# Optimization experiments

Measured on AMD Instinct MI355X. Metric: run time of the kernel, lower is better.

The kernel has to match this reference:

```python
import jax, jax.numpy as jnp
import numpy as np

N, IN_DIM, HID, E = 2048, 128, 64, 32768
EPS = 1e-5  # torch BatchNorm1d / LayerNorm default eps


def setup_inputs() -> dict:
    key = jax.random.key(0)
    ks = jax.random.split(key, 12)
    s = 0.05
    return {
        "h": jax.random.normal(ks[0], (N, IN_DIM), jnp.float32),
        "local": jax.random.normal(ks[1], (N, IN_DIM), jnp.float32),
        "e": jax.random.normal(ks[2], (E, HID), jnp.float32),
        "src": jax.random.randint(ks[3], (E,), 0, N, jnp.int32),
        "dst": jax.random.randint(ks[4], (E,), 0, N, jnp.int32),
        "ln_w": jnp.ones((IN_DIM,), jnp.float32),
        "ln_b": jnp.zeros((IN_DIM,), jnp.float32),
        "conv_w": jax.random.normal(ks[5], (1, 2, 3), jnp.float32) * 0.3,
        "conv_b": jnp.zeros((1,), jnp.float32),
        "W1": jax.random.normal(ks[6], (IN_DIM, HID * HID), jnp.float32) * s,
        "b1": jnp.zeros((HID * HID,), jnp.float32),
        "Wp2": jax.random.normal(ks[7], (IN_DIM, HID), jnp.float32) * s,
        "bp2": jnp.zeros((HID,), jnp.float32),
        "W2": jax.random.normal(ks[8], (IN_DIM, HID), jnp.float32) * s,
        "b2": jnp.zeros((HID,), jnp.float32),
        "W3": jax.random.normal(ks[9], (HID, HID), jnp.float32) * s,
        "b3": jnp.zeros((HID,), jnp.float32),
        "bng_g": jnp.ones((HID,), jnp.float32),
        "bng_b": jnp.zeros((HID,), jnp.float32),
        "bnG_g": jnp.ones((HID,), jnp.float32),
        "bnG_b": jnp.zeros((HID,), jnp.float32),
        "bnL_g": jnp.ones((HID,), jnp.float32),
        "bnL_b": jnp.zeros((HID,), jnp.float32),
    }


def _bn_eval(x, g, b):
    # BatchNorm1d in eval mode, running_mean=0, running_var=1
    return x * (g / jnp.sqrt(1.0 + EPS)) + b


def _layernorm(x, w, b):
    mu = jnp.mean(x, axis=-1, keepdims=True)
    var = jnp.var(x, axis=-1, keepdims=True)
    return (x - mu) / jnp.sqrt(var + EPS) * w + b


def reference(h, local, e, src, dst, ln_w, ln_b, conv_w, conv_b,
              W1, b1, Wp2, bp2, W2, b2, W3, b3,
              bng_g, bng_b, bnG_g, bnG_b, bnL_g, bnL_b):
    # ---- local edge branch ----
    edge = jnp.stack([local[src], local[dst]], axis=1)  # [E, 2, in_dim]
    edge = _layernorm(edge, ln_w, ln_b)
    # Conv1d(2 -> 1, k=3, pad=1) over the in_dim axis
    lr_local = jax.lax.conv_general_dilated(
        edge, conv_w, window_strides=(1,), padding=[(1, 1)],
        dimension_numbers=("NCH", "OIH", "NCH"))[:, 0, :] + conv_b  # [E, in_dim]
    lr_local = jax.nn.relu(lr_local)  # dropout is identity in eval
    lr_local = lr_local @ W2 + b2  # [E, hid]

    # ---- global edge branch ----
    p1 = jax.nn.relu(h @ W1 + b1).reshape(h.shape[0], HID, HID)  # [N, hid(d), hid(k)]
    p2 = jax.nn.relu(h @ Wp2 + bp2)  # [N, hid(k)]
    # mm[i, j, d] = sum_k p1[i, d, k] * p2[j, k]; gather only needed edges
    lr_global = jnp.einsum("edk,ek->ed", p1[src], p2[dst])  # [E, hid]
    lr_global = _bn_eval(lr_global, bng_g, bng_b) @ W3 + b3
    lr_global = jax.nn.relu(_bn_eval(lr_global, bnG_g, bnG_b))

    lr_local = jax.nn.relu(_bn_eval(lr_local, bnL_g, bnL_b))
    return lr_local + lr_global + e
```

## Files before the change

### kernel.cpp

```cpp
#include <hip/hip_runtime.h>

#define N_NODES 2048
#define IN_DIM 128
#define HID 64
#define N_EDGES 32768
#define EPS 1e-5f
#define CAP 64
#define TPN 4
#define NTILES (N_NODES * TPN)
#define POISON ((int)0xAAAAAAAA)

typedef short short8 __attribute__((ext_vector_type(8)));
typedef float f32x4 __attribute__((ext_vector_type(4)));

__device__ __forceinline__ float relu_f(float x) { return fmaxf(x, 0.f); }

__device__ __forceinline__ unsigned short f2bf(float f) {
  unsigned int u = __float_as_uint(f);
  u = (u + 0x7fffu + ((u >> 16) & 1u)) >> 16;
  return (unsigned short)u;
}
__device__ __forceinline__ float bf2f(unsigned short h) {
  return __uint_as_float(((unsigned int)h) << 16);
}
__device__ __forceinline__ short8 pack8(const float* f) {
  short8 o;
  #pragma unroll
  for (int i = 0; i < 8; ++i) o[i] = (short)f2bf(f[i]);
  return o;
}

__global__ __launch_bounds__(256) void gemm_prep(
    const float* __restrict__ h, const float* __restrict__ local,
    const float* __restrict__ ln_w, const float* __restrict__ ln_b,
    const float* __restrict__ Wp2, const float* __restrict__ bp2,
    const float* __restrict__ W1, const float* __restrict__ b1,
    const float* __restrict__ W2, const float* __restrict__ W3,
    const int* __restrict__ src, const int* __restrict__ dst,
    unsigned short* __restrict__ p1b, unsigned short* __restrict__ lnlb,
    unsigned short* __restrict__ p2b,
    unsigned short* __restrict__ w2tb, unsigned short* __restrict__ w3tb,
    int* __restrict__ cursor, int2* __restrict__ slot_ed)
{
  __shared__ __align__(16) struct { float hs[4][IN_DIM]; } S;
  const int b = blockIdx.x, t = threadIdx.x;
  const int w = t >> 6, l = t & 63;
  const int lr = l & 15, lq = l >> 4;

  if (b < 1024) {
    const int bm = (b & 31) * 64;
    const int bn = (b >> 5) * 128;
    const int m0 = bm + w * 16;
    f32x4 acc[8];
    #pragma unroll
    for (int ni = 0; ni < 8; ++ni) acc[ni] = (f32x4){0.f, 0.f, 0.f, 0.f};

    #pragma unroll
    for (int k0 = 0; k0 < 128; k0 += 32) {
      const float* hrow = h + (size_t)(m0 + lr) * 128 + k0 + lq * 8;
      float4 h0 = *(const float4*)hrow;
      float4 h1 = *(const float4*)(hrow + 4);
      short8 bmf;
      bmf[0] = (short)f2bf(h0.x); bmf[1] = (short)f2bf(h0.y);
      bmf[2] = (short)f2bf(h0.z); bmf[3] = (short)f2bf(h0.w);
      bmf[4] = (short)f2bf(h1.x); bmf[5] = (short)f2bf(h1.y);
      bmf[6] = (short)f2bf(h1.z); bmf[7] = (short)f2bf(h1.w);
      const float* wcol = W1 + (size_t)(k0 + lq * 8) * 4096 + bn + lr;
      #pragma unroll
      for (int ni = 0; ni < 8; ++ni) {
        short8 a;
        #pragma unroll
        for (int j = 0; j < 8; ++j)
          a[j] = (short)f2bf(wcol[(size_t)j * 4096 + ni * 16]);
        acc[ni] = __builtin_amdgcn_mfma_f32_16x16x32_bf16(a, bmf, acc[ni], 0, 0, 0);
      }
    }
    const int m = m0 + lr;
    #pragma unroll
    for (int ni = 0; ni < 8; ++ni) {
      int n = bn + ni * 16 + lq * 4;
      float4 bv = *(const float4*)&b1[n];
      ushort4 o;
      o.x = f2bf(relu_f(acc[ni][0] + bv.x));
      o.y = f2bf(relu_f(acc[ni][1] + bv.y));
      o.z = f2bf(relu_f(acc[ni][2] + bv.z));
      o.w = f2bf(relu_f(acc[ni][3] + bv.w));
      *(ushort4*)&p1b[(size_t)m * 4096 + n] = o;
    }
    return;
  }

  const int pb = b - 1024;
  if (pb < 128) {
    #pragma unroll
    for (int i = 0; i < 4; ++i) {
      int row = pb * 16 + w * 4 + i;
      const float* x = local + (size_t)row * IN_DIM;
      float x0 = x[l], x1 = x[l + 64];
      float s1 = x0 + x1, s2 = x0 * x0 + x1 * x1;
      #pragma unroll
      for (int off = 32; off > 0; off >>= 1) {
        s1 += __shfl_xor(s1, off);
        s2 += __shfl_xor(s2, off);
      }
      float mean = s1 * (1.f / IN_DIM);
      float var = s2 * (1.f / IN_DIM) - mean * mean;
      float rstd = rsqrtf(var + EPS);
      unsigned short* o = lnlb + (size_t)row * IN_DIM;
      o[l]      = f2bf((x0 - mean) * rstd * ln_w[l] + ln_b[l]);
      o[l + 64] = f2bf((x1 - mean) * rstd * ln_w[l + 64] + ln_b[l + 64]);
    }
  } else if (pb < 256) {
    int qb = pb - 128;
    #pragma unroll
    for (int i = 0; i < 4; ++i) {
      int row = qb * 16 + w * 4 + i;
      S.hs[w][l] = h[(size_t)row * IN_DIM + l];
      S.hs[w][l + 64] = h[(size_t)row * IN_DIM + 64 + l];
      float acc = bp2[l];
      #pragma unroll 8
      for (int m = 0; m < IN_DIM; ++m) acc += S.hs[w][m] * Wp2[m * HID + l];
      p2b[(size_t)row * HID + l] = f2bf(relu_f(acc));
    }
  } else if (pb == 256) {
    for (int i = t; i < IN_DIM * HID; i += 256) {
      int x = i >> 6, j = i & 63;
      w2tb[j * IN_DIM + x] = f2bf(W2[i]);
    }
  } else if (pb == 257) {
    for (int i = t; i < HID * HID; i += 256) {
      int k = i >> 6, j = i & 63;
      w3tb[j * HID + k] = f2bf(W3[i]);
    }
  } else {
    int base = (pb - 258) * 512;
    #pragma unroll
    for (int it = 0; it < 2; ++it) {
      int e = base + it * 256 + t;
      int s = src[e];
      int r = atomicAdd(&cursor[s], 1) - POISON;
      if (r < CAP) slot_ed[s * CAP + r] = make_int2(e, dst[e]);
    }
  }
}

__global__ __launch_bounds__(256, 6) void edge_mfma(
    const unsigned short* __restrict__ p1b, const unsigned short* __restrict__ p2b,
    const unsigned short* __restrict__ lnlb,
    const int2* __restrict__ slot_ed,
    const unsigned short* __restrict__ w2tb, const unsigned short* __restrict__ w3tb,
    const float* __restrict__ conv_w, const float* __restrict__ conv_b,
    const float* __restrict__ b2, const float* __restrict__ b3,
    const float* __restrict__ bng_g, const float* __restrict__ bng_b,
    const float* __restrict__ bnG_g, const float* __restrict__ bnG_b,
    const float* __restrict__ bnL_g, const float* __restrict__ bnL_b,
    const float* __restrict__ e_in, float* __restrict__ out)
{
  __shared__ float gs[4][16][68];

  const int t = threadIdx.x;
  const int w = t >> 6, l = t & 63;
  const int lr = l & 15, lq = l >> 4;
  const float rs = rsqrtf(1.f + EPS);

  const int tile = blockIdx.x * 4 + w;
  const int srcn = tile >> 2;

  const int2 ed = slot_ed[tile * 16 + lr];

  const unsigned short* rows = lnlb + (size_t)srcn * IN_DIM;
  short8 ach[4];
  #pragma unroll
  for (int ks = 0; ks < 4; ++ks)
    ach[ks] = *(const short8*)(rows + ks * 32 + lq * 8);
  const unsigned short* pr = p1b + (size_t)srcn * 4096 + lr * 64 + lq * 8;

  if (!__any(ed.x >= 0)) return;
  const int eidx = ed.x;
  const int dn = (eidx >= 0) ? ed.y : 0;

  const unsigned short* rowd = lnlb + (size_t)dn * IN_DIM;
  short8 bch[4];
  #pragma unroll
  for (int ks = 0; ks < 4; ++ks)
    bch[ks] = *(const short8*)(rowd + ks * 32 + lq * 8);
  const unsigned short* p2r = p2b + (size_t)dn * HID + lq * 8;
  short8 a0 = *(const short8*)(p2r);
  short8 a1 = *(const short8*)(p2r + 32);

  f32x4 c[4];
  #pragma unroll
  for (int ni = 0; ni < 4; ++ni) {
    c[ni] = (f32x4){0.f, 0.f, 0.f, 0.f};
    short8 pb0 = *(const short8*)(pr + ni * 1024);
    short8 pb1 = *(const short8*)(pr + ni * 1024 + 32);
    c[ni] = __builtin_amdgcn_mfma_f32_16x16x32_bf16(a0, pb0, c[ni], 0, 0, 0);
    c[ni] = __builtin_amdgcn_mfma_f32_16x16x32_bf16(a1, pb1, c[ni], 0, 0, 0);
  }

  #pragma unroll
  for (int ni = 0; ni < 4; ++ni) {
    int col = ni * 16 + lr;
    float g = bng_g[col] * rs, bb = bng_b[col];
    #pragma unroll
    for (int r = 0; r < 4; ++r)
      gs[w][lq * 4 + r][ni * 16 + lr] = c[ni][r] * g + bb;
  }

  const float cw0 = conv_w[0], cw1 = conv_w[1], cw2 = conv_w[2];
  const float cw3 = conv_w[3], cw4 = conv_w[4], cw5 = conv_w[5];
  const float cb = conv_b[0];
  float aL[4], aR[4], bL[4], bR[4];
  #pragma unroll
  for (int ks = 0; ks < 4; ++ks) {
    int kL = ks * 32 + lq * 8 - 1;
    int kR = ks * 32 + lq * 8 + 8;
    bool vL = (kL >= 0), vR = (kR < IN_DIM);
    aL[ks] = vL ? bf2f(rows[kL]) : 0.f;
    bL[ks] = vL ? bf2f(rowd[kL]) : 0.f;
    aR[ks] = vR ? bf2f(rows[kR]) : 0.f;
    bR[ks] = vR ? bf2f(rowd[kR]) : 0.f;
  }
  f32x4 v[4];
  #pragma unroll
  for (int ni = 0; ni < 4; ++ni) v[ni] = (f32x4){0.f, 0.f, 0.f, 0.f};
  #pragma unroll
  for (int ks = 0; ks < 4; ++ks) {
    float A[8], B[8];
    #pragma unroll
    for (int j = 0; j < 8; ++j) {
      A[j] = bf2f((unsigned short)ach[ks][j]);
      B[j] = bf2f((unsigned short)bch[ks][j]);
    }
    short8 af;
    #pragma unroll
    for (int j = 0; j < 8; ++j) {
      float am = j ? A[j - 1] : aL[ks];
      float ap = (j < 7) ? A[j + 1] : aR[ks];
      float bm = j ? B[j - 1] : bL[ks];
      float bp = (j < 7) ? B[j + 1] : bR[ks];
      float cv = relu_f(cw0 * am + cw1 * A[j] + cw2 * ap +
                        cw3 * bm + cw4 * B[j] + cw5 * bp + cb);
      af[j] = (short)f2bf(cv);
    }
    #pragma unroll
    for (int ni = 0; ni < 4; ++ni) {
      short8 wb = *(const short8*)(w2tb + (size_t)(ni * 16 + lr) * IN_DIM + ks * 32 + lq * 8);
      v[ni] = __builtin_amdgcn_mfma_f32_16x16x32_bf16(af, wb, v[ni], 0, 0, 0);
    }
  }

  asm volatile("s_waitcnt lgkmcnt(0)" ::: "memory");
  short8 ga0 = pack8(&gs[w][lr][lq * 8]);
  short8 ga1 = pack8(&gs[w][lr][32 + lq * 8]);

  const unsigned short* wr3 = w3tb + lr * HID + lq * 8;
  f32x4 u[4];
  #pragma unroll
  for (int ni = 0; ni < 4; ++ni) {
    u[ni] = (f32x4){0.f, 0.f, 0.f, 0.f};
    short8 wb0 = *(const short8*)(wr3 + ni * 1024);
    short8 wb1 = *(const short8*)(wr3 + ni * 1024 + 32);
    u[ni] = __builtin_amdgcn_mfma_f32_16x16x32_bf16(ga0, wb0, u[ni], 0, 0, 0);
    u[ni] = __builtin_amdgcn_mfma_f32_16x16x32_bf16(ga1, wb1, u[ni], 0, 0, 0);
  }

  int er[4];
  #pragma unroll
  for (int r = 0; r < 4; ++r) er[r] = __shfl(eidx, lq * 4 + r);
  #pragma unroll
  for (int ni = 0; ni < 4; ++ni) {
    int col = ni * 16 + lr;
    float gG = bnG_g[col] * rs, bG = bnG_b[col];
    float gL = bnL_g[col] * rs, bbL = bnL_b[col];
    float c3 = b3[col], c2 = b2[col];
    #pragma unroll
    for (int r = 0; r < 4; ++r) {
      int e = er[r];
      if (e >= 0) {
        float vg = relu_f((u[ni][r] + c3) * gG + bG);
        float vl = relu_f((v[ni][r] + c2) * gL + bbL);
        out[(size_t)e * HID + col] = vl + vg + e_in[(size_t)e * HID + col];
      }
    }
  }
}

extern "C" void kernel_launch(void* const* d_in, const int* in_sizes, int n_in,
                              void* d_out, int out_size, void* d_ws, size_t ws_size,
                              hipStream_t stream) {
  const float* h      = (const float*)d_in[0];
  const float* local  = (const float*)d_in[1];
  const float* e_in   = (const float*)d_in[2];
  const int*   src    = (const int*)d_in[3];
  const int*   dst    = (const int*)d_in[4];
  const float* ln_w   = (const float*)d_in[5];
  const float* ln_b   = (const float*)d_in[6];
  const float* conv_w = (const float*)d_in[7];
  const float* conv_b = (const float*)d_in[8];
  const float* W1     = (const float*)d_in[9];
  const float* b1     = (const float*)d_in[10];
  const float* Wp2    = (const float*)d_in[11];
  const float* bp2    = (const float*)d_in[12];
  const float* W2     = (const float*)d_in[13];
  const float* b2     = (const float*)d_in[14];
  const float* W3     = (const float*)d_in[15];
  const float* b3     = (const float*)d_in[16];
  const float* bng_g  = (const float*)d_in[17];
  const float* bng_b  = (const float*)d_in[18];
  const float* bnG_g  = (const float*)d_in[19];
  const float* bnG_b  = (const float*)d_in[20];
  const float* bnL_g  = (const float*)d_in[21];
  const float* bnL_b  = (const float*)d_in[22];
  float* out = (float*)d_out;

  char* p = (char*)d_ws;
  unsigned short* p1b  = (unsigned short*)p; p += (size_t)N_NODES * HID * HID * 2;
  unsigned short* p2b  = (unsigned short*)p; p += (size_t)N_NODES * HID * 2;
  unsigned short* lnlb = (unsigned short*)p; p += (size_t)N_NODES * IN_DIM * 2;
  unsigned short* w2tb = (unsigned short*)p; p += (size_t)HID * IN_DIM * 2;
  unsigned short* w3tb = (unsigned short*)p; p += (size_t)HID * HID * 2;
  int*  cursor  = (int*)p;  p += N_NODES * 4;
  int2* slot_ed = (int2*)p; p += (size_t)NTILES * 16 * 8;


  gemm_prep<<<1346, 256, 0, stream>>>(h, local, ln_w, ln_b, Wp2, bp2, W1, b1, W2, W3,
                                      src, dst, p1b, lnlb, p2b, w2tb, w3tb,
                                      cursor, slot_ed);
  edge_mfma<<<2048, 256, 0, stream>>>(p1b, p2b, lnlb, slot_ed,
                                      w2tb, w3tb, conv_w, conv_b, b2, b3,
                                      bng_g, bng_b, bnG_g, bnG_b, bnL_g, bnL_b, e_in, out);
}
```

Measured before the change: 164.1 us.

## Stage W1 tile in LDS as bf16 and double M tile per GEMM block

```diff
diff --git a/kernel.cpp b/kernel.cpp
--- a/kernel.cpp
+++ b/kernel.cpp
@@ -42,55 +42,77 @@
     unsigned short* __restrict__ w2tb, unsigned short* __restrict__ w3tb,
     int* __restrict__ cursor, int2* __restrict__ slot_ed)
 {
-  __shared__ __align__(16) struct { float hs[4][IN_DIM]; } S;
+  __shared__ __align__(16) union {
+    unsigned short wlds[128 * 136];
+    float hs[4][IN_DIM];
+  } S;
   const int b = blockIdx.x, t = threadIdx.x;
   const int w = t >> 6, l = t & 63;
   const int lr = l & 15, lq = l >> 4;
 
-  if (b < 1024) {
-    const int bm = (b & 31) * 64;
-    const int bn = (b >> 5) * 128;
-    const int m0 = bm + w * 16;
-    f32x4 acc[8];
-    #pragma unroll
-    for (int ni = 0; ni < 8; ++ni) acc[ni] = (f32x4){0.f, 0.f, 0.f, 0.f};
+  if (b < 512) {
+    const int bm = (b & 15) * 128;
+    const int bn = (b >> 4) * 128;
+
+    #pragma unroll
+    for (int it = 0; it < 16; ++it) {
+      int flat = it * 1024 + t * 4;
+      int k = flat >> 7, n = flat & 127;
+      float4 v = *(const float4*)&W1[(size_t)k * 4096 + bn + n];
+      S.wlds[(n + 0) * 136 + k] = f2bf(v.x);
+      S.wlds[(n + 1) * 136 + k] = f2bf(v.y);
+      S.wlds[(n + 2) * 136 + k] = f2bf(v.z);
+      S.wlds[(n + 3) * 136 + k] = f2bf(v.w);
+    }
+    __syncthreads();
+
+    const int m0 = bm + w * 32;
+    f32x4 acc[2][8];
+    #pragma unroll
+    for (int mi = 0; mi < 2; ++mi)
+      #pragma unroll
+      for (int ni = 0; ni < 8; ++ni) acc[mi][ni] = (f32x4){0.f, 0.f, 0.f, 0.f};
 
     #pragma unroll
     for (int k0 = 0; k0 < 128; k0 += 32) {
-      const float* hrow = h + (size_t)(m0 + lr) * 128 + k0 + lq * 8;
-      float4 h0 = *(const float4*)hrow;
-      float4 h1 = *(const float4*)(hrow + 4);
-      short8 bmf;
-      bmf[0] = (short)f2bf(h0.x); bmf[1] = (short)f2bf(h0.y);
-      bmf[2] = (short)f2bf(h0.z); bmf[3] = (short)f2bf(h0.w);
-      bmf[4] = (short)f2bf(h1.x); bmf[5] = (short)f2bf(h1.y);
-      bmf[6] = (short)f2bf(h1.z); bmf[7] = (short)f2bf(h1.w);
-      const float* wcol = W1 + (size_t)(k0 + lq * 8) * 4096 + bn + lr;
+      short8 bmf[2];
+      #pragma unroll
+      for (int mi = 0; mi < 2; ++mi) {
+        const float* hrow = h + (size_t)(m0 + mi * 16 + lr) * 128 + k0 + lq * 8;
+        float4 h0 = *(const float4*)hrow;
+        float4 h1 = *(const float4*)(hrow + 4);
+        bmf[mi][0] = (short)f2bf(h0.x); bmf[mi][1] = (short)f2bf(h0.y);
+        bmf[mi][2] = (short)f2bf(h0.z); bmf[mi][3] = (short)f2bf(h0.w);
+        bmf[mi][4] = (short)f2bf(h1.x); bmf[mi][5] = (short)f2bf(h1.y);
+        bmf[mi][6] = (short)f2bf(h1.z); bmf[mi][7] = (short)f2bf(h1.w);
+      }
       #pragma unroll
       for (int ni = 0; ni < 8; ++ni) {
-        short8 a;
+        short8 a = *(const short8*)&S.wlds[(ni * 16 + lr) * 136 + k0 + lq * 8];
         #pragma unroll
-        for (int j = 0; j < 8; ++j)
-          a[j] = (short)f2bf(wcol[(size_t)j * 4096 + ni * 16]);
-        acc[ni] = __builtin_amdgcn_mfma_f32_16x16x32_bf16(a, bmf, acc[ni], 0, 0, 0);
-      }
-    }
-    const int m = m0 + lr;
-    #pragma unroll
-    for (int ni = 0; ni < 8; ++ni) {
-      int n = bn + ni * 16 + lq * 4;
-      float4 bv = *(const float4*)&b1[n];
-      ushort4 o;
-      o.x = f2bf(relu_f(acc[ni][0] + bv.x));
-      o.y = f2bf(relu_f(acc[ni][1] + bv.y));
-      o.z = f2bf(relu_f(acc[ni][2] + bv.z));
-      o.w = f2bf(relu_f(acc[ni][3] + bv.w));
-      *(ushort4*)&p1b[(size_t)m * 4096 + n] = o;
+        for (int mi = 0; mi < 2; ++mi)
+          acc[mi][ni] = __builtin_amdgcn_mfma_f32_16x16x32_bf16(a, bmf[mi], acc[mi][ni], 0, 0, 0);
+      }
+    }
+    #pragma unroll
+    for (int mi = 0; mi < 2; ++mi) {
+      const int m = m0 + mi * 16 + lr;
+      #pragma unroll
+      for (int ni = 0; ni < 8; ++ni) {
+        int n = bn + ni * 16 + lq * 4;
+        float4 bv = *(const float4*)&b1[n];
+        ushort4 o;
+        o.x = f2bf(relu_f(acc[mi][ni][0] + bv.x));
+        o.y = f2bf(relu_f(acc[mi][ni][1] + bv.y));
+        o.z = f2bf(relu_f(acc[mi][ni][2] + bv.z));
+        o.w = f2bf(relu_f(acc[mi][ni][3] + bv.w));
+        *(ushort4*)&p1b[(size_t)m * 4096 + n] = o;
+      }
     }
     return;
   }
 
-  const int pb = b - 1024;
+  const int pb = b - 512;
   if (pb < 128) {
     #pragma unroll
     for (int i = 0; i < 4; ++i) {
@@ -324,9 +346,9 @@
   int2* slot_ed = (int2*)p; p += (size_t)NTILES * 16 * 8;
 
 
-  gemm_prep<<<1346, 256, 0, stream>>>(h, local, ln_w, ln_b, Wp2, bp2, W1, b1, W2, W3,
-                                      src, dst, p1b, lnlb, p2b, w2tb, w3tb,
-                                      cursor, slot_ed);
+  gemm_prep<<<834, 256, 0, stream>>>(h, local, ln_w, ln_b, Wp2, bp2, W1, b1, W2, W3,
+                                     src, dst, p1b, lnlb, p2b, w2tb, w3tb,
+                                     cursor, slot_ed);
   edge_mfma<<<2048, 256, 0, stream>>>(p1b, p2b, lnlb, slot_ed,
                                       w2tb, w3tb, conv_w, conv_b, b2, b3,
                                       bng_g, bng_b, bnG_g, bnG_b, bnL_g, bnL_b, e_in, out);
```

Result: faster. 160.4 us (-2.3%).
